# Optimization experiments

Hardware: AMD Instinct MI355X
Metric: run time of the kernel (lower is better)

The kernel has to match this reference:

```python
import jax, jax.numpy as jnp
import numpy as np

N = 50000        # number of nodes
E = 1600000      # number of (directed) edges, ~degree 32
D = 128          # latent_dim
L = 2            # num_layers
NEG_SLOPE = 0.01 # torch F.leaky_relu default


def setup_inputs() -> dict:
    key = jax.random.key(0)
    k1, k2, k3, k4 = jax.random.split(key, 4)
    h = jax.random.normal(k1, (N, D), dtype=jnp.float32)
    src = jax.random.randint(k2, (E,), 0, N, dtype=jnp.int32)
    dst = jax.random.randint(k3, (E,), 0, N, dtype=jnp.int32)
    # attn_fc per layer: Linear(2*D, 1, bias=False) -> weight vector of length 2*D
    att_w = jax.random.normal(k4, (L, 2 * D), dtype=jnp.float32) * 0.1
    return {"h": h, "src": src, "dst": dst, "att_w": att_w}


def _segment_softmax(e, seg, n):
    # numerically-stable softmax over edges grouped by destination node
    m = jax.ops.segment_max(e, seg, num_segments=n)      # [N]
    ex = jnp.exp(e - m[seg])                             # [E]
    s = jax.ops.segment_sum(ex, seg, num_segments=n)     # [N]
    return ex / s[seg]


def reference(h, src, dst, att_w):
    n, d = h.shape
    for l in range(att_w.shape[0]):
        w_src = att_w[l, :d]   # weight applied to edges.src['h']
        w_dst = att_w[l, d:]   # weight applied to edges.dst['h']
        # a = attn_fc(concat(h_src, h_dst)) = h_src @ w_src + h_dst @ w_dst
        a = h[src] @ w_src + h[dst] @ w_dst               # [E]
        e = jnp.where(a > 0, a, NEG_SLOPE * a)            # leaky_relu
        alpha = _segment_softmax(e, dst, n)               # edge_softmax by dst
        # update_all: m = h_src * e ; h_dst = sum(m)
        h = jax.ops.segment_sum(h[src] * alpha[:, None], dst, num_segments=n)
    return h
```

## Files before the change

### kernel.cpp

```cpp
#include <hip/hip_runtime.h>
#include <hip/hip_fp16.h>
#include <math.h>

#define NEG_SLOPE 0.01f
#define BKT_BITS 7
#define BKT_MASK 127
#define SBLOCKS  256
#define STPB     512


__global__ void bkhist_kernel(const int* __restrict__ dst, int* __restrict__ blockhist,
                              int E, int NB, int chunk) {
    extern __shared__ int lh[];
    for (int k = threadIdx.x; k < NB; k += blockDim.x) lh[k] = 0;
    __syncthreads();
    int b = blockIdx.x;
    int beg = b * chunk, end = min(E, beg + chunk);
    for (int e = beg + (int)threadIdx.x; e < end; e += blockDim.x)
        atomicAdd(&lh[dst[e] >> BKT_BITS], 1);
    __syncthreads();
    for (int k = threadIdx.x; k < NB; k += blockDim.x)
        blockhist[k * SBLOCKS + b] = lh[k];
}

__global__ void scan1_kernel(const int* __restrict__ in, int* __restrict__ local_excl,
                             int* __restrict__ partials, int n) {
    __shared__ int sm[1024];
    int i = blockIdx.x * 1024 + threadIdx.x;
    int x = (i < n) ? in[i] : 0;
    sm[threadIdx.x] = x;
    __syncthreads();
    for (int off = 1; off < 1024; off <<= 1) {
        int y = (threadIdx.x >= (unsigned)off) ? sm[threadIdx.x - off] : 0;
        __syncthreads();
        sm[threadIdx.x] += y;
        __syncthreads();
    }
    if (i < n) local_excl[i] = sm[threadIdx.x] - x;
    if (threadIdx.x == 1023) partials[blockIdx.x] = sm[1023];
}

__global__ void scan2_kernel(int* __restrict__ partials, int nchunks) {
    __shared__ int sm[1024];
    int x = (threadIdx.x < (unsigned)nchunks) ? partials[threadIdx.x] : 0;
    sm[threadIdx.x] = x;
    __syncthreads();
    for (int off = 1; off < 1024; off <<= 1) {
        int y = (threadIdx.x >= (unsigned)off) ? sm[threadIdx.x - off] : 0;
        __syncthreads();
        sm[threadIdx.x] += y;
        __syncthreads();
    }
    partials[threadIdx.x] = sm[threadIdx.x] - x;
    if (threadIdx.x == 1023) partials[1024] = sm[1023];
}

__global__ void scan3_kernel(const int* __restrict__ local_excl, const int* __restrict__ partials,
                             int* __restrict__ out, int n) {
    int i = blockIdx.x * 1024 + threadIdx.x;
    if (i < n) out[i] = local_excl[i] + partials[blockIdx.x];
    if (i == n) out[n] = partials[1024];
}

__global__ void bksplit_kernel(const int* __restrict__ src, const int* __restrict__ dst,
                               const int* __restrict__ bh_scan, unsigned* __restrict__ pairs,
                               int E, int NB, int chunk) {
    extern __shared__ int lm[];
    int* lbase = lm;
    int* lcnt  = lm + NB;
    int b = blockIdx.x;
    for (int k = threadIdx.x; k < NB; k += blockDim.x) {
        lbase[k] = bh_scan[k * SBLOCKS + b];
        lcnt[k]  = 0;
    }
    __syncthreads();
    int beg = b * chunk, end = min(E, beg + chunk);
    for (int e = beg + (int)threadIdx.x; e < end; e += blockDim.x) {
        int d = dst[e];
        int k = d >> BKT_BITS;
        int pos = lbase[k] + atomicAdd(&lcnt[k], 1);
        pairs[pos] = ((unsigned)src[e] << BKT_BITS) | (unsigned)(d & BKT_MASK);
    }
}

__global__ void csr_build_kernel(const unsigned* __restrict__ pairs, const int* __restrict__ bh_scan,
                                 int* __restrict__ row_ptr, int* __restrict__ csr_src,
                                 int E, int N, int NB) {
    __shared__ int ldeg[128];
    __shared__ int lscan[128];
    __shared__ int lpos[128];
    int k = blockIdx.x;
    int bbase = bh_scan[k * SBLOCKS];
    int bend  = bh_scan[(k + 1) * SBLOCKS];
    if (threadIdx.x < 128) ldeg[threadIdx.x] = 0;
    __syncthreads();
    for (int i = bbase + (int)threadIdx.x; i < bend; i += blockDim.x)
        atomicAdd(&ldeg[pairs[i] & BKT_MASK], 1);
    __syncthreads();
    int x = (threadIdx.x < 128) ? ldeg[threadIdx.x] : 0;
    if (threadIdx.x < 128) lscan[threadIdx.x] = x;
    __syncthreads();
    for (int off = 1; off < 128; off <<= 1) {
        int y = 0;
        if (threadIdx.x < 128 && threadIdx.x >= (unsigned)off) y = lscan[threadIdx.x - off];
        __syncthreads();
        if (threadIdx.x < 128) lscan[threadIdx.x] += y;
        __syncthreads();
    }
    if (threadIdx.x < 128) {
        int excl = lscan[threadIdx.x] - x;
        int node = (k << BKT_BITS) + threadIdx.x;
        if (node < N) row_ptr[node] = bbase + excl;
        lpos[threadIdx.x] = excl;
    }
    if (k == NB - 1 && threadIdx.x == 0) row_ptr[N] = E;
    __syncthreads();
    for (int i = bbase + (int)threadIdx.x; i < bend; i += blockDim.x) {
        unsigned p = pairs[i];
        int pos = atomicAdd(&lpos[p & BKT_MASK], 1);
        csr_src[bbase + pos] = (int)(p >> BKT_BITS);
    }
}


__global__ void stconv_kernel(const float* __restrict__ h, const float* __restrict__ att_w_l,
                              float* __restrict__ s, float* __restrict__ t,
                              __half* __restrict__ h16, int n) {
    int gid  = blockIdx.x * blockDim.x + threadIdx.x;
    int v    = gid >> 6;
    int lane = threadIdx.x & 63;
    if (v >= n) return;
    float2 hv = ((const float2*)(h + (size_t)v * 128))[lane];
    ((__half2*)(h16 + (size_t)v * 128))[lane] = __floats2half2_rn(hv.x, hv.y);
    float2 ws = ((const float2*)att_w_l)[lane];
    float2 wd = ((const float2*)(att_w_l + 128))[lane];
    float ps = hv.x * ws.x + hv.y * ws.y;
    float pt = hv.x * wd.x + hv.y * wd.y;
    for (int off = 32; off > 0; off >>= 1) {
        ps += __shfl_down(ps, off);
        pt += __shfl_down(pt, off);
    }
    if (lane == 0) { s[v] = ps; t[v] = pt; }
}

__device__ __forceinline__ void gath(const __half* __restrict__ hin, int uu, float wgt,
                                     int hlane, float4& acc) {
    float2 r = ((const float2*)(hin + (size_t)uu * 128))[hlane];
    float2 f01 = __half22float2(*(const __half2*)&r.x);
    float2 f23 = __half22float2(*(const __half2*)&r.y);
    acc.x = fmaf(wgt, f01.x, acc.x); acc.y = fmaf(wgt, f01.y, acc.y);
    acc.z = fmaf(wgt, f23.x, acc.z); acc.w = fmaf(wgt, f23.y, acc.w);
}

template<bool LAST>
__global__ void agg_kernel(const __half* __restrict__ hin, const float* __restrict__ s,
                           const float* __restrict__ t, const int* __restrict__ row_ptr,
                           const int* __restrict__ csr_src,
                           __half* __restrict__ hout16, float* __restrict__ outf,
                           const float* __restrict__ att_w_next,
                           float* __restrict__ s2, float* __restrict__ t2, int n) {
    int gid   = blockIdx.x * blockDim.x + threadIdx.x;
    int v     = gid >> 6;
    int lane  = threadIdx.x & 63;
    if (v >= n) return;
    int half  = lane >> 5;
    int hlane = lane & 31;

    int beg = row_ptr[v];
    int end = row_ptr[v + 1];
    float tv = t[v];

    float4 acc = make_float4(0.f, 0.f, 0.f, 0.f);
    float lsum_l = 0.f;

    for (int base = beg; base < end; base += 64) {
        int cnt = end - base;
        if (cnt > 64) cnt = 64;
        int idx = base + min(lane, cnt - 1);
        int u   = csr_src[idx];
        float a = s[u] + tv;
        float e = (a > 0.f) ? a : NEG_SLOPE * a;
        float wl = (lane < cnt) ? __expf(e) : 0.f;
        lsum_l += wl;
        int steps = (cnt + 1) >> 1;
        int k = 0;
        for (; k + 1 < steps; k += 2) {
            int sl0 = (k << 1) + half;
            int sl1 = (k << 1) + 2 + half;
            int   u0 = __shfl(u, sl0);
            float w0 = __shfl(wl, sl0);
            int   u1 = __shfl(u, sl1);
            float w1 = __shfl(wl, sl1);
            gath(hin, u0, w0, hlane, acc);
            gath(hin, u1, w1, hlane, acc);
        }
        if (k < steps) {
            int sl = (k << 1) + half;
            int   u0 = __shfl(u, sl);
            float w0 = __shfl(wl, sl);
            gath(hin, u0, w0, hlane, acc);
        }
    }
    float lsum = lsum_l;
    for (int off = 32; off > 0; off >>= 1) lsum += __shfl_xor(lsum, off);
    acc.x += __shfl_xor(acc.x, 32);
    acc.y += __shfl_xor(acc.y, 32);
    acc.z += __shfl_xor(acc.z, 32);
    acc.w += __shfl_xor(acc.w, 32);
    float inv_l = (lsum > 0.f) ? (1.0f / lsum) : 0.f;
    acc.x *= inv_l; acc.y *= inv_l; acc.z *= inv_l; acc.w *= inv_l;

    if (LAST) {
        if (half == 0)
            ((float4*)(outf + (size_t)v * 128))[hlane] = acc;
    } else {
        if (half == 0) {
            __half2 q01 = __floats2half2_rn(acc.x, acc.y);
            __half2 q23 = __floats2half2_rn(acc.z, acc.w);
            float2 packed;
            packed.x = *(const float*)&q01;
            packed.y = *(const float*)&q23;
            ((float2*)(hout16 + (size_t)v * 128))[hlane] = packed;
        }
        float4 ws4 = ((const float4*)att_w_next)[hlane];
        float4 wd4 = ((const float4*)(att_w_next + 128))[hlane];
        float ps = acc.x * ws4.x + acc.y * ws4.y + acc.z * ws4.z + acc.w * ws4.w;
        float pt = acc.x * wd4.x + acc.y * wd4.y + acc.z * wd4.z + acc.w * wd4.w;
        for (int off = 16; off > 0; off >>= 1) {
            ps += __shfl_down(ps, off);
            pt += __shfl_down(pt, off);
        }
        if (lane == 0) { s2[v] = ps; t2[v] = pt; }
    }
}


extern "C" void kernel_launch(void* const* d_in, const int* in_sizes, int n_in,
                              void* d_out, int out_size, void* d_ws, size_t ws_size,
                              hipStream_t stream) {
    const float* h0    = (const float*)d_in[0];
    const int*   src   = (const int*)d_in[1];
    const int*   dst   = (const int*)d_in[2];
    const float* att_w = (const float*)d_in[3];
    int N = in_sizes[0] / 128;
    int E = in_sizes[1];
    int L = in_sizes[3] / 256;
    float* out = (float*)d_out;

    int NB = (N + BKT_MASK) >> BKT_BITS;
    int n2 = NB * SBLOCKS;
    int chunk = (E + SBLOCKS - 1) / SBLOCKS;
    int nch2 = (n2 + 1023) / 1024;

    char* ws = (char*)d_ws;
    size_t off = 0;
    auto alloc = [&](size_t bytes) -> void* {
        void* p = ws + off;
        off = (off + bytes + 511) & ~(size_t)511;
        return p;
    };
    int*      row_ptr   = (int*)     alloc((size_t)(N + 1) * 4);
    int*      csr_src   = (int*)     alloc((size_t)E * 4);
    float*    s1        = (float*)   alloc((size_t)N * 4);
    float*    t1        = (float*)   alloc((size_t)N * 4);
    float*    s2        = (float*)   alloc((size_t)N * 4);
    float*    t2        = (float*)   alloc((size_t)N * 4);
    __half*   hA        = (__half*)  alloc((size_t)N * 128 * 2);
    __half*   hB        = (__half*)  alloc((size_t)N * 128 * 2);
    unsigned* pairs     = (unsigned*)alloc((size_t)E * 4);
    int*      blockhist = (int*)     alloc((size_t)n2 * 4);
    int*      bh_scan   = (int*)     alloc((size_t)(n2 + 1) * 4);
    int*      local_ex  = (int*)     alloc((size_t)n2 * 4);
    int*      partials  = (int*)     alloc(1025 * 4);

    bkhist_kernel<<<SBLOCKS, STPB, NB * 4, stream>>>(dst, blockhist, E, NB, chunk);
    scan1_kernel<<<nch2, 1024, 0, stream>>>(blockhist, local_ex, partials, n2);
    scan2_kernel<<<1, 1024, 0, stream>>>(partials, nch2);
    scan3_kernel<<<nch2, 1024, 0, stream>>>(local_ex, partials, bh_scan, n2);
    bksplit_kernel<<<SBLOCKS, STPB, 2 * NB * 4, stream>>>(src, dst, bh_scan, pairs, E, NB, chunk);
    csr_build_kernel<<<NB, 512, 0, stream>>>(pairs, bh_scan, row_ptr, csr_src, E, N, NB);

    const int tb = 256;
    int node_blocks = (N * 64 + tb - 1) / tb;

    stconv_kernel<<<node_blocks, tb, 0, stream>>>(h0, att_w, s1, t1, hA, N);

    __half* hin = hA;
    __half* hnx = hB;
    float *sc = s1, *tc = t1, *sn = s2, *tn = t2;
    for (int l = 0; l < L; ++l) {
        if (l == L - 1) {
            agg_kernel<true><<<node_blocks, tb, 0, stream>>>(
                hin, sc, tc, row_ptr, csr_src, nullptr, out, nullptr, nullptr, nullptr, N);
        } else {
            agg_kernel<false><<<node_blocks, tb, 0, stream>>>(
                hin, sc, tc, row_ptr, csr_src, hnx, nullptr,
                att_w + (size_t)(l + 1) * 256, sn, tn, N);
            __half* tmp = hin; hin = hnx; hnx = tmp;
            float* tf;
            tf = sc; sc = sn; sn = tf;
            tf = tc; tc = tn; tn = tf;
        }
    }
}
```

Measured before the change: 238.2 us.

## Fuse preprocessing kernels to cut launches in CSR build

Merges the node projection and fp16 conversion into the dst histogram kernel. The three-kernel scan becomes a single kernel that uses a last-block-done atomic to compute chunk offsets. Bucket offsets are then taken as local_ex plus coff at use sites instead of materialising a full scanned array. The aim is fewer kernel launches and less inter-kernel idle time, at the cost of a grid-stride stconv loop over only 256 blocks and fixed shared arrays that cap NB at 512.

```diff
diff --git a/kernel.cpp b/kernel.cpp
--- a/kernel.cpp
+++ b/kernel.cpp
@@ -5,27 +5,47 @@
 #define NEG_SLOPE 0.01f
 #define BKT_BITS 7
 #define BKT_MASK 127
-#define SBLOCKS  256
-#define STPB     512
-
-
-__global__ void bkhist_kernel(const int* __restrict__ dst, int* __restrict__ blockhist,
-                              int E, int NB, int chunk) {
-    extern __shared__ int lh[];
-    for (int k = threadIdx.x; k < NB; k += blockDim.x) lh[k] = 0;
-    __syncthreads();
-    int b = blockIdx.x;
+#define PG   256
+#define PT   512
+
+__global__ void __launch_bounds__(PT) stconv_hist_kernel(
+        const float* __restrict__ h0, const float* __restrict__ att_w,
+        float* __restrict__ s1, float* __restrict__ t1, __half* __restrict__ hA,
+        const int* __restrict__ dst, int* __restrict__ blockhist, int* __restrict__ done,
+        int N, int E, int NB, int chunk) {
+    __shared__ int lh[512];
+    int b = blockIdx.x, tid = threadIdx.x;
+    if (b == 0 && tid == 0) *done = 0;
+    {
+        int lane = tid & 63;
+        float2 wsv = ((const float2*)att_w)[lane];
+        float2 wdv = ((const float2*)(att_w + 128))[lane];
+        for (int v = b * (PT / 64) + (tid >> 6); v < N; v += PG * (PT / 64)) {
+            float2 hv = ((const float2*)(h0 + (size_t)v * 128))[lane];
+            ((__half2*)(hA + (size_t)v * 128))[lane] = __floats2half2_rn(hv.x, hv.y);
+            float ps = hv.x * wsv.x + hv.y * wsv.y;
+            float pt = hv.x * wdv.x + hv.y * wdv.y;
+            for (int off = 32; off > 0; off >>= 1) {
+                ps += __shfl_down(ps, off);
+                pt += __shfl_down(pt, off);
+            }
+            if (lane == 0) { s1[v] = ps; t1[v] = pt; }
+        }
+    }
+    for (int k = tid; k < NB; k += PT) lh[k] = 0;
+    __syncthreads();
     int beg = b * chunk, end = min(E, beg + chunk);
-    for (int e = beg + (int)threadIdx.x; e < end; e += blockDim.x)
+    for (int e = beg + tid; e < end; e += PT)
         atomicAdd(&lh[dst[e] >> BKT_BITS], 1);
     __syncthreads();
-    for (int k = threadIdx.x; k < NB; k += blockDim.x)
-        blockhist[k * SBLOCKS + b] = lh[k];
-}
-
-__global__ void scan1_kernel(const int* __restrict__ in, int* __restrict__ local_excl,
-                             int* __restrict__ partials, int n) {
+    for (int k = tid; k < NB; k += PT) blockhist[k * PG + b] = lh[k];
+}
+
+__global__ void scan12_kernel(const int* __restrict__ in, int* __restrict__ local_excl,
+                              int* __restrict__ partials, int* __restrict__ coff,
+                              int* __restrict__ done, int n, int nch) {
     __shared__ int sm[1024];
+    __shared__ int amlast;
     int i = blockIdx.x * 1024 + threadIdx.x;
     int x = (i < n) ? in[i] : 0;
     sm[threadIdx.x] = x;
@@ -38,12 +58,14 @@
     }
     if (i < n) local_excl[i] = sm[threadIdx.x] - x;
     if (threadIdx.x == 1023) partials[blockIdx.x] = sm[1023];
-}
-
-__global__ void scan2_kernel(int* __restrict__ partials, int nchunks) {
-    __shared__ int sm[1024];
-    int x = (threadIdx.x < (unsigned)nchunks) ? partials[threadIdx.x] : 0;
-    sm[threadIdx.x] = x;
+    __threadfence();
+    __syncthreads();
+    if (threadIdx.x == 0) amlast = (atomicAdd(done, 1) == nch - 1);
+    __syncthreads();
+    if (!amlast) return;
+    __threadfence();
+    int p = (threadIdx.x < (unsigned)nch) ? partials[threadIdx.x] : 0;
+    sm[threadIdx.x] = p;
     __syncthreads();
     for (int off = 1; off < 1024; off <<= 1) {
         int y = (threadIdx.x >= (unsigned)off) ? sm[threadIdx.x - off] : 0;
@@ -51,31 +73,25 @@
         sm[threadIdx.x] += y;
         __syncthreads();
     }
-    partials[threadIdx.x] = sm[threadIdx.x] - x;
-    if (threadIdx.x == 1023) partials[1024] = sm[1023];
-}
-
-__global__ void scan3_kernel(const int* __restrict__ local_excl, const int* __restrict__ partials,
-                             int* __restrict__ out, int n) {
-    int i = blockIdx.x * 1024 + threadIdx.x;
-    if (i < n) out[i] = local_excl[i] + partials[blockIdx.x];
-    if (i == n) out[n] = partials[1024];
-}
-
-__global__ void bksplit_kernel(const int* __restrict__ src, const int* __restrict__ dst,
-                               const int* __restrict__ bh_scan, unsigned* __restrict__ pairs,
-                               int E, int NB, int chunk) {
-    extern __shared__ int lm[];
-    int* lbase = lm;
-    int* lcnt  = lm + NB;
-    int b = blockIdx.x;
-    for (int k = threadIdx.x; k < NB; k += blockDim.x) {
-        lbase[k] = bh_scan[k * SBLOCKS + b];
+    if (threadIdx.x < (unsigned)nch) coff[threadIdx.x] = sm[threadIdx.x] - p;
+    if (threadIdx.x == 1023) coff[nch] = sm[1023];
+}
+
+__global__ void __launch_bounds__(PT) bksplit_kernel(
+        const int* __restrict__ src, const int* __restrict__ dst,
+        const int* __restrict__ local_ex, const int* __restrict__ coff,
+        unsigned* __restrict__ pairs, int E, int NB, int chunk) {
+    __shared__ int lbase[512];
+    __shared__ int lcnt[512];
+    int b = blockIdx.x, tid = threadIdx.x;
+    for (int k = tid; k < NB; k += PT) {
+        int idx = k * PG + b;
+        lbase[k] = local_ex[idx] + coff[idx >> 10];
         lcnt[k]  = 0;
     }
     __syncthreads();
     int beg = b * chunk, end = min(E, beg + chunk);
-    for (int e = beg + (int)threadIdx.x; e < end; e += blockDim.x) {
+    for (int e = beg + tid; e < end; e += PT) {
         int d = dst[e];
         int k = d >> BKT_BITS;
         int pos = lbase[k] + atomicAdd(&lcnt[k], 1);
@@ -83,65 +99,49 @@
     }
 }
 
-__global__ void csr_build_kernel(const unsigned* __restrict__ pairs, const int* __restrict__ bh_scan,
+__global__ void csr_build_kernel(const unsigned* __restrict__ pairs,
+                                 const int* __restrict__ local_ex, const int* __restrict__ coff,
                                  int* __restrict__ row_ptr, int* __restrict__ csr_src,
                                  int E, int N, int NB) {
     __shared__ int ldeg[128];
     __shared__ int lscan[128];
     __shared__ int lpos[128];
-    int k = blockIdx.x;
-    int bbase = bh_scan[k * SBLOCKS];
-    int bend  = bh_scan[(k + 1) * SBLOCKS];
-    if (threadIdx.x < 128) ldeg[threadIdx.x] = 0;
-    __syncthreads();
-    for (int i = bbase + (int)threadIdx.x; i < bend; i += blockDim.x)
+    int k = blockIdx.x, tid = threadIdx.x;
+    int i0 = k * PG;
+    int bbase = local_ex[i0] + coff[i0 >> 10];
+    int bend;
+    if (k == NB - 1) bend = E;
+    else { int i1 = (k + 1) * PG; bend = local_ex[i1] + coff[i1 >> 10]; }
+    if (tid < 128) ldeg[tid] = 0;
+    __syncthreads();
+    for (int i = bbase + tid; i < bend; i += blockDim.x)
         atomicAdd(&ldeg[pairs[i] & BKT_MASK], 1);
     __syncthreads();
-    int x = (threadIdx.x < 128) ? ldeg[threadIdx.x] : 0;
-    if (threadIdx.x < 128) lscan[threadIdx.x] = x;
+    int x = (tid < 128) ? ldeg[tid] : 0;
+    if (tid < 128) lscan[tid] = x;
     __syncthreads();
     for (int off = 1; off < 128; off <<= 1) {
         int y = 0;
-        if (threadIdx.x < 128 && threadIdx.x >= (unsigned)off) y = lscan[threadIdx.x - off];
-        __syncthreads();
-        if (threadIdx.x < 128) lscan[threadIdx.x] += y;
-        __syncthreads();
-    }
-    if (threadIdx.x < 128) {
-        int excl = lscan[threadIdx.x] - x;
-        int node = (k << BKT_BITS) + threadIdx.x;
+        if (tid < 128 && tid >= off) y = lscan[tid - off];
+        __syncthreads();
+        if (tid < 128) lscan[tid] += y;
+        __syncthreads();
+    }
+    if (tid < 128) {
+        int excl = lscan[tid] - x;
+        int node = (k << BKT_BITS) + tid;
         if (node < N) row_ptr[node] = bbase + excl;
-        lpos[threadIdx.x] = excl;
-    }
-    if (k == NB - 1 && threadIdx.x == 0) row_ptr[N] = E;
-    __syncthreads();
-    for (int i = bbase + (int)threadIdx.x; i < bend; i += blockDim.x) {
+        lpos[tid] = excl;
+    }
+    if (k == NB - 1 && tid == 0) row_ptr[N] = E;
+    __syncthreads();
+    for (int i = bbase + tid; i < bend; i += blockDim.x) {
         unsigned p = pairs[i];
         int pos = atomicAdd(&lpos[p & BKT_MASK], 1);
         csr_src[bbase + pos] = (int)(p >> BKT_BITS);
     }
 }
 
-
-__global__ void stconv_kernel(const float* __restrict__ h, const float* __restrict__ att_w_l,
-                              float* __restrict__ s, float* __restrict__ t,
-                              __half* __restrict__ h16, int n) {
-    int gid  = blockIdx.x * blockDim.x + threadIdx.x;
-    int v    = gid >> 6;
-    int lane = threadIdx.x & 63;
-    if (v >= n) return;
-    float2 hv = ((const float2*)(h + (size_t)v * 128))[lane];
-    ((__half2*)(h16 + (size_t)v * 128))[lane] = __floats2half2_rn(hv.x, hv.y);
-    float2 ws = ((const float2*)att_w_l)[lane];
-    float2 wd = ((const float2*)(att_w_l + 128))[lane];
-    float ps = hv.x * ws.x + hv.y * ws.y;
-    float pt = hv.x * wd.x + hv.y * wd.y;
-    for (int off = 32; off > 0; off >>= 1) {
-        ps += __shfl_down(ps, off);
-        pt += __shfl_down(pt, off);
-    }
-    if (lane == 0) { s[v] = ps; t[v] = pt; }
-}
 
 __device__ __forceinline__ void gath(const __half* __restrict__ hin, int uu, float wgt,
                                      int hlane, float4& acc) {
@@ -248,9 +248,9 @@
     float* out = (float*)d_out;
 
     int NB = (N + BKT_MASK) >> BKT_BITS;
-    int n2 = NB * SBLOCKS;
-    int chunk = (E + SBLOCKS - 1) / SBLOCKS;
-    int nch2 = (n2 + 1023) / 1024;
+    int n2 = NB * PG;
+    int chunk = (E + PG - 1) / PG;
+    int nch = (n2 + 1023) / 1024;
 
     char* ws = (char*)d_ws;
     size_t off = 0;
@@ -269,21 +269,19 @@
     __half*   hB        = (__half*)  alloc((size_t)N * 128 * 2);
     unsigned* pairs     = (unsigned*)alloc((size_t)E * 4);
     int*      blockhist = (int*)     alloc((size_t)n2 * 4);
-    int*      bh_scan   = (int*)     alloc((size_t)(n2 + 1) * 4);
     int*      local_ex  = (int*)     alloc((size_t)n2 * 4);
-    int*      partials  = (int*)     alloc(1025 * 4);
-
-    bkhist_kernel<<<SBLOCKS, STPB, NB * 4, stream>>>(dst, blockhist, E, NB, chunk);
-    scan1_kernel<<<nch2, 1024, 0, stream>>>(blockhist, local_ex, partials, n2);
-    scan2_kernel<<<1, 1024, 0, stream>>>(partials, nch2);
-    scan3_kernel<<<nch2, 1024, 0, stream>>>(local_ex, partials, bh_scan, n2);
-    bksplit_kernel<<<SBLOCKS, STPB, 2 * NB * 4, stream>>>(src, dst, bh_scan, pairs, E, NB, chunk);
-    csr_build_kernel<<<NB, 512, 0, stream>>>(pairs, bh_scan, row_ptr, csr_src, E, N, NB);
+    int*      partials  = (int*)     alloc((size_t)(nch + 1) * 4);
+    int*      coff      = (int*)     alloc((size_t)(nch + 1) * 4);
+    int*      done      = (int*)     alloc(4);
+
+    stconv_hist_kernel<<<PG, PT, 0, stream>>>(h0, att_w, s1, t1, hA,
+                                              dst, blockhist, done, N, E, NB, chunk);
+    scan12_kernel<<<nch, 1024, 0, stream>>>(blockhist, local_ex, partials, coff, done, n2, nch);
+    bksplit_kernel<<<PG, PT, 0, stream>>>(src, dst, local_ex, coff, pairs, E, NB, chunk);
+    csr_build_kernel<<<NB, 512, 0, stream>>>(pairs, local_ex, coff, row_ptr, csr_src, E, N, NB);
 
     const int tb = 256;
     int node_blocks = (N * 64 + tb - 1) / tb;
-
-    stconv_kernel<<<node_blocks, tb, 0, stream>>>(h0, att_w, s1, t1, hA, N);
 
     __half* hin = hA;
     __half* hnx = hB;
```

After: 275.4 us. +15.6%, slower.
